# Performance work log

Measured on AMD Instinct MI355X. Metric: run time of the kernel, lower is better.

The kernel has to match this reference:

```python
import jax, jax.numpy as jnp
import numpy as np

BATCH = 16384
NUM_FIELDS = 20
NUM_FEATURES = 100000
LATENT_DIM = 64


def setup_inputs() -> dict:
    key = jax.random.key(0)
    k_x, k_e = jax.random.split(key)
    x = jax.random.randint(k_x, (BATCH, NUM_FIELDS), 0, NUM_FEATURES, dtype=jnp.int32)
    field_indices = jnp.arange(NUM_FIELDS, dtype=jnp.int32)
    # one embedding table per field, stacked: [F, num_features, D]
    emb = jax.random.normal(k_e, (NUM_FIELDS, NUM_FEATURES, LATENT_DIM), dtype=jnp.float32)
    return {"x": x, "field_indices": field_indices, "emb": emb}


def reference(x, field_indices, emb):
    # linear part: sum of raw integer indices over fields (as in the torch code)
    linear = jnp.sum(x, axis=1).astype(emb.dtype)  # [B]
    F = emb.shape[0]
    # gather v_i = emb[i][x[:, i]] for all fields at once -> [B, F, D]
    V = emb[jnp.arange(F)[None, :], x]
    # sum_{i<j} <v_i, v_j> = 0.5 * (||sum_i v_i||^2 - sum_i ||v_i||^2)
    s = jnp.sum(V, axis=1)                           # [B, D]
    interaction = 0.5 * (jnp.sum(s * s, axis=-1) - jnp.sum(V * V, axis=(1, 2)))  # [B]
    return linear + interaction
```

## Files before the change

### kernel.cpp

```cpp
#include <hip/hip_runtime.h>


constexpr int BATCH = 16384;
constexpr int NUM_FIELDS = 20;
constexpr int NUM_FEATURES = 100000;
constexpr int LATENT = 64;

__global__ __launch_bounds__(256)
void ffm_kernel(const int* __restrict__ x,
                const float* __restrict__ emb,
                float* __restrict__ out) {
    const int wave_in_block = threadIdx.x >> 6;
    const int lane          = threadIdx.x & 63;
    const int row           = blockIdx.x * 4 + wave_in_block;
    if (row >= BATCH) return;

    const int* xr = x + row * NUM_FIELDS;

    float s    = 0.0f;
    float sq   = 0.0f;
    float xsum = 0.0f;

#pragma unroll
    for (int f = 0; f < NUM_FIELDS; ++f) {
        const int idx = xr[f];
        xsum += (float)idx;
        const int off = (f * NUM_FEATURES + idx) * LATENT + lane;
        const float v = emb[off];
        s  += v;
        sq += v * v;
    }

    float t = 0.5f * (s * s - sq);

#pragma unroll
    for (int off = 32; off > 0; off >>= 1)
        t += __shfl_down(t, off, 64);

    if (lane == 0)
        out[row] = xsum + t;
}

extern "C" void kernel_launch(void* const* d_in, const int* in_sizes, int n_in,
                              void* d_out, int out_size, void* d_ws, size_t ws_size,
                              hipStream_t stream) {
    const int*   x   = (const int*)d_in[0];
    const float* emb = (const float*)d_in[2];
    float*       out = (float*)d_out;

    const int rows_per_block = 4;
    const int grid = (BATCH + rows_per_block - 1) / rows_per_block;
    ffm_kernel<<<grid, 256, 0, stream>>>(x, emb, out);
}
```

Measured before the change: 562.9 us.

## Split gather into field-major gather kernel plus per-row reduce kernel via workspace

Replaces the fused per-row kernel with two kernels when a workspace is available. The first gathers embedding rows field by field, so consecutive blocks touch one table at a time, and writes them to an intermediate [B,F,D] buffer. The second reads that buffer back and computes the interaction plus the index sum. This aims to improve locality of the random embedding reads, but it adds an 84 MB write and read of the intermediate buffer and a second kernel launch.

Result: slower. 586.8 us (+4.2%).

```diff
diff --git a/kernel.cpp b/kernel.cpp
--- a/kernel.cpp
+++ b/kernel.cpp
@@ -6,10 +6,65 @@
 constexpr int NUM_FEATURES = 100000;
 constexpr int LATENT = 64;
 
+constexpr int ROWS_PER_WAVE_A = 4;
+constexpr int ROWS_PER_BLOCK_A = 4 * ROWS_PER_WAVE_A;
+constexpr int CHUNKS_PER_FIELD = BATCH / ROWS_PER_BLOCK_A;
+
 __global__ __launch_bounds__(256)
-void ffm_kernel(const int* __restrict__ x,
-                const float* __restrict__ emb,
-                float* __restrict__ out) {
+void gather_kernel(const int* __restrict__ x,
+                   const float* __restrict__ emb,
+                   float* __restrict__ V) {
+    const int wave = threadIdx.x >> 6;
+    const int lane = threadIdx.x & 63;
+    const int f     = blockIdx.x >> 10;
+    const int chunk = blockIdx.x & 1023;
+    const int r0 = chunk * ROWS_PER_BLOCK_A + wave * ROWS_PER_WAVE_A;
+
+    const float* __restrict__ ef = emb + (size_t)f * NUM_FEATURES * LATENT;
+
+#pragma unroll
+    for (int g = 0; g < ROWS_PER_WAVE_A; ++g) {
+        const int row = r0 + g;
+        const int idx = x[row * NUM_FIELDS + f];
+        const float v = ef[idx * LATENT + lane];
+        V[((size_t)row * NUM_FIELDS + f) * LATENT + lane] = v;
+    }
+}
+
+__global__ __launch_bounds__(256)
+void reduce_kernel(const int* __restrict__ x,
+                   const float* __restrict__ V,
+                   float* __restrict__ out) {
+    const int wave = threadIdx.x >> 6;
+    const int lane = threadIdx.x & 63;
+    const int row  = blockIdx.x * 4 + wave;
+
+    const float* __restrict__ vr = V + (size_t)row * NUM_FIELDS * LATENT;
+
+    float s = 0.0f, sq = 0.0f;
+#pragma unroll
+    for (int f = 0; f < NUM_FIELDS; ++f) {
+        const float v = vr[f * LATENT + lane];
+        s  += v;
+        sq += v * v;
+    }
+    float t = 0.5f * (s * s - sq);
+
+    if (lane < NUM_FIELDS)
+        t += (float)x[row * NUM_FIELDS + lane];
+
+#pragma unroll
+    for (int off = 32; off > 0; off >>= 1)
+        t += __shfl_down(t, off, 64);
+
+    if (lane == 0)
+        out[row] = t;
+}
+
+__global__ __launch_bounds__(256)
+void ffm_fused_kernel(const int* __restrict__ x,
+                      const float* __restrict__ emb,
+                      float* __restrict__ out) {
     const int wave_in_block = threadIdx.x >> 6;
     const int lane          = threadIdx.x & 63;
     const int row           = blockIdx.x * 4 + wave_in_block;
@@ -17,10 +72,7 @@
 
     const int* xr = x + row * NUM_FIELDS;
 
-    float s    = 0.0f;
-    float sq   = 0.0f;
-    float xsum = 0.0f;
-
+    float s = 0.0f, sq = 0.0f, xsum = 0.0f;
 #pragma unroll
     for (int f = 0; f < NUM_FIELDS; ++f) {
         const int idx = xr[f];
@@ -30,13 +82,10 @@
         s  += v;
         sq += v * v;
     }
-
     float t = 0.5f * (s * s - sq);
-
 #pragma unroll
     for (int off = 32; off > 0; off >>= 1)
         t += __shfl_down(t, off, 64);
-
     if (lane == 0)
         out[row] = xsum + t;
 }
@@ -48,7 +97,14 @@
     const float* emb = (const float*)d_in[2];
     float*       out = (float*)d_out;
 
-    const int rows_per_block = 4;
-    const int grid = (BATCH + rows_per_block - 1) / rows_per_block;
-    ffm_kernel<<<grid, 256, 0, stream>>>(x, emb, out);
+    const size_t v_bytes = (size_t)BATCH * NUM_FIELDS * LATENT * sizeof(float);
+
+    if (d_ws != nullptr && ws_size >= v_bytes) {
+        float* V = (float*)d_ws;
+        gather_kernel<<<NUM_FIELDS * CHUNKS_PER_FIELD, 256, 0, stream>>>(x, emb, V);
+        reduce_kernel<<<BATCH / 4, 256, 0, stream>>>(x, V, out);
+    } else {
+        const int grid = (BATCH + 3) / 4;
+        ffm_fused_kernel<<<grid, 256, 0, stream>>>(x, emb, out);
+    }
 }
```
